# Kernel tuning notes

Hardware: AMD Instinct MI355X
Metric: run time of the kernel (lower is better)

The kernel has to match this reference:

```python
import jax, jax.numpy as jnp
import numpy as np

NUM_HEAD = 16
NUM_SEQ = 2048
NUM_FEAT = 1024
HEAD_DIM = NUM_FEAT // NUM_HEAD
LN_EPS = 1e-5


def _constants():
    # decay per head: log(1 - 2^{-5-h})
    decay = jnp.log(1.0 - 2.0 ** (-5.0 - jnp.arange(NUM_HEAD, dtype=jnp.float32)))
    idx = jnp.arange(NUM_SEQ, dtype=jnp.float32)
    diff = idx[:, None] - idx[None, :]                      # [s, s]
    # exp(diff * decay) on lower triangle (incl. diagonal), 0 above
    mask = jnp.where(diff[None] >= 0, jnp.exp(diff[None] * decay[:, None, None]), 0.0)  # [h, s, s]
    # rotary angles: each frequency repeated twice
    angle = 1.0 / 10000.0 ** jnp.linspace(0.0, 1.0, HEAD_DIM // 2)
    angle = jnp.repeat(angle, 2)                            # [hd]
    sin = jnp.sin(idx[:, None] * angle[None, :])            # [s, hd]
    cos = jnp.cos(idx[:, None] * angle[None, :])
    return mask, sin, cos


def _rotate_every_two(x):
    x1 = x[..., ::2]
    x2 = x[..., 1::2]
    return jnp.stack((-x2, x1), axis=-1).reshape(x.shape)


def setup_inputs() -> dict:
    key = jax.random.key(0)
    ks = jax.random.split(key, 5)
    b, s, d = 4, NUM_SEQ, NUM_FEAT
    x = jax.random.normal(ks[0], (b, s, d), dtype=jnp.float32)
    Wq = jax.random.normal(ks[1], (d, d), dtype=jnp.float32) * 0.02
    Wk = jax.random.normal(ks[2], (d, d), dtype=jnp.float32) * 0.02
    Wv = jax.random.normal(ks[3], (d, d), dtype=jnp.float32) * 0.02
    Wo = jax.random.normal(ks[4], (d, d), dtype=jnp.float32) * 0.02
    ln_w = jnp.ones((HEAD_DIM,), dtype=jnp.float32)
    ln_b = jnp.zeros((HEAD_DIM,), dtype=jnp.float32)
    return {"x": x, "Wq": Wq, "Wk": Wk, "Wv": Wv, "Wo": Wo, "ln_w": ln_w, "ln_b": ln_b}


def reference(x, Wq, Wk, Wv, Wo, ln_w, ln_b):
    b, s, d = x.shape
    h, hd = NUM_HEAD, HEAD_DIM
    mask, sin, cos = _constants()

    def proj(W):
        # torch Linear (no bias): x @ W.T -> [b, h, s, hd]
        return (x @ W.T).reshape(b, s, h, hd).transpose(0, 2, 1, 3)

    q, k, v = proj(Wq), proj(Wk), proj(Wv)
    # rotary theta shift (sin/cos broadcast over batch & head)
    q = q * cos + _rotate_every_two(q) * sin
    k = k * cos + _rotate_every_two(k) * sin

    r = jnp.einsum('bhsd,bhtd->bhst', q, k) * mask[None]    # decay-masked scores
    o = jnp.einsum('bhst,bhtd->bhsd', r, v)                 # [b, h, s, hd]

    # LayerNorm over head_dim
    mu = jnp.mean(o, axis=-1, keepdims=True)
    var = jnp.var(o, axis=-1, keepdims=True)
    y = (o - mu) * jax.lax.rsqrt(var + LN_EPS) * ln_w + ln_b

    y = y.transpose(0, 2, 1, 3).reshape(b, s, d)
    return jax.nn.silu(y) @ Wo.T
```

## Files before the change

### kernel.cpp

```cpp
#include <hip/hip_runtime.h>
#include <math.h>

typedef unsigned short u16;
typedef __attribute__((ext_vector_type(8))) short short8;
typedef __attribute__((ext_vector_type(4))) float floatx4;

#define LDS_AS(p) ((__attribute__((address_space(3))) void*)(p))
#define GLB_AS(p) ((const __attribute__((address_space(1))) void*)(p))

__device__ __forceinline__ u16 f2bf(float f) {
  unsigned int u = __float_as_uint(f);
  u += 0x7fffu + ((u >> 16) & 1u);
  return (u16)(u >> 16);
}

__device__ __forceinline__ void gld16(const void* g, void* l) {
  __builtin_amdgcn_global_load_lds(GLB_AS(g), LDS_AS(l), 16, 0, 0);
}

__device__ __forceinline__ floatx4 mfma16(short8 a, short8 b, floatx4 c) {
  return __builtin_amdgcn_mfma_f32_16x16x32_bf16(a, b, c, 0, 0, 0);
}

__global__ void prep_kernel(const float* __restrict__ x, const float* __restrict__ Wq,
                            const float* __restrict__ Wk, const float* __restrict__ Wv,
                            const float* __restrict__ Wo, u16* __restrict__ xbf,
                            u16* __restrict__ wqkv, u16* __restrict__ wo,
                            float2* __restrict__ rtab) {
  int i = blockIdx.x * blockDim.x + threadIdx.x;
  const int str = gridDim.x * blockDim.x;
  for (; i < 3211264; i += str) {
    if (i < 3145728) {
      const float* s; u16* d; int j;
      if (i < 2097152)      { s = x;  d = xbf;            j = i; }
      else if (i < 2359296) { s = Wq; d = wqkv;           j = i - 2097152; }
      else if (i < 2621440) { s = Wk; d = wqkv + 1048576; j = i - 2359296; }
      else if (i < 2883584) { s = Wv; d = wqkv + 2097152; j = i - 2621440; }
      else                  { s = Wo; d = wo;             j = i - 2883584; }
      float4 v = ((const float4*)s)[j];
      ushort4 o;
      o.x = f2bf(v.x); o.y = f2bf(v.y); o.z = f2bf(v.z); o.w = f2bf(v.w);
      ((ushort4*)d)[j] = o;
    } else {
      const int t = i - 3145728;
      const int seq = t >> 5, dh = t & 31;
      const float freq = exp2f(-(float)dh * 0.42863594770f);
      float sn, cs;
      __sincosf((float)seq * freq, &sn, &cs);
      rtab[t] = make_float2(sn, cs);
    }
  }
}

template <int EPI>
__global__ __launch_bounds__(512, 4)
void gemm_bt(const u16* __restrict__ A, const u16* __restrict__ Bw, int K,
             u16* __restrict__ qb, u16* __restrict__ kb, u16* __restrict__ vtb,
             u16* __restrict__ kwt, const float2* __restrict__ rtab,
             float* __restrict__ outp) {
  __shared__ __align__(16) u16 smem[36864];
  const int tid = threadIdx.x;
  const int w = tid >> 6, lane = tid & 63;
  const int quad = lane >> 4, l15 = lane & 15;
  const int wr = w >> 2, wc = w & 3;
  const int m0 = blockIdx.y * 128, n0 = blockIdx.x * 256;

  const u16* Ag = A + (size_t)(m0 + w * 16 + l15) * K + quad * 8;
  const u16* Bg = Bw + (size_t)(n0 + 2 * w * 16 + l15) * K + quad * 8;
  const size_t row16 = (size_t)16 * K;

  auto stage = [&](int buf, int k0) {
    const int nb = buf * 12288;
    gld16(Ag + k0, &smem[nb + w * 512]);
#pragma unroll
    for (int e = 0; e < 2; ++e)
      gld16(Bg + e * row16 + k0, &smem[nb + 4096 + (2 * w + e) * 512]);
  };

  floatx4 acc[4][4] = {};
  const int NT = K >> 5;

  stage(0, 0);
  stage(1, 32);

  int cur = 0, stg = 2;
  for (int t = 0; t < NT; ++t) {
    if (t + 1 < NT)
      asm volatile("s_waitcnt vmcnt(3)" ::: "memory");
    else
      asm volatile("s_waitcnt vmcnt(0)" ::: "memory");
    __builtin_amdgcn_s_barrier();
    asm volatile("" ::: "memory");
    __builtin_amdgcn_sched_barrier(0);

    if (t + 2 < NT) stage(stg, (t + 2) * 32);

    const u16* Ap = &smem[cur * 12288];
    const u16* Bp = &smem[cur * 12288 + 4096];
    short8 a[4], b[4];
#pragma unroll
    for (int i = 0; i < 4; ++i)
      a[i] = *(const short8*)&Ap[(wr * 4 + i) * 512 + lane * 8];
#pragma unroll
    for (int j = 0; j < 4; ++j)
      b[j] = *(const short8*)&Bp[(wc * 4 + j) * 512 + lane * 8];
    __builtin_amdgcn_s_setprio(1);
#pragma unroll
    for (int i = 0; i < 4; ++i)
#pragma unroll
      for (int j = 0; j < 4; ++j)
        acc[i][j] = mfma16(a[i], b[j], acc[i][j]);
    __builtin_amdgcn_s_setprio(0);
    asm volatile("" ::: "memory");
    cur = (cur == 2) ? 0 : cur + 1;
    stg = (stg == 2) ? 0 : stg + 1;
  }
  __builtin_amdgcn_s_barrier();

  u16* scr = &smem[w * 4096];

  const int mrb = m0 + wr * 64;
  const int ncb = n0 + wc * 64;

  if (EPI == 0) {
    const int which = n0 >> 10;
    const int c1024 = ncb & 1023;
    const int bidx = mrb >> 11;
    const int hh = c1024 >> 6;
    const int seq0 = mrb & 2047;
    const int lr = lane >> 3, lc = lane & 7;

    if (which < 2) {
#pragma unroll
      for (int j = 0; j < 4; ++j) {
        const int d = j * 16 + l15;
        const int dc = d >> 3, dl = d & 7;
#pragma unroll
        for (int i = 0; i < 4; ++i)
#pragma unroll
          for (int r = 0; r < 4; ++r) {
            const int sl = i * 16 + quad * 4 + r;
            const int seq = seq0 + sl;
            const float v = acc[i][j][r];
            const float p = __shfl_xor(v, 1, 64);
            const float2 sc = rtab[(d >> 1) + seq * 32];
            const float res = (d & 1) ? (v * sc.y + p * sc.x) : (v * sc.y - p * sc.x);
            scr[sl * 64 + (((dc + (sl >> 2)) & 7) << 3) + dl] = f2bf(res);
          }
      }
      u16* dst = ((which == 0) ? qb : kb) + (size_t)(bidx * 16 + hh) * 131072 +
                 (size_t)seq0 * 64;
#pragma unroll
      for (int cch = 0; cch < 8; ++cch) {
        const int row = cch * 8 + lr;
        const int slot = (lc + (row >> 2)) & 7;
        short8 vv = *(const short8*)&scr[row * 64 + slot * 8];
        *(short8*)(dst + (size_t)row * 64 + lc * 8) = vv;
      }
      if (which == 1) {
        const float l2h = __log2f(1.0f - exp2f(-(float)(5 + hh)));
#pragma unroll
        for (int j = 0; j < 4; ++j) {
          const int d = j * 16 + l15;
#pragma unroll
          for (int i = 0; i < 4; ++i) {
            ushort4 pk;
#pragma unroll
            for (int r = 0; r < 4; ++r) {
              const int sl = i * 16 + quad * 4 + r;
              const int seq = seq0 + sl;
              const float v = acc[i][j][r];
              const float p = __shfl_xor(v, 1, 64);
              const float2 sc = rtab[(d >> 1) + seq * 32];
              const float res = (d & 1) ? (v * sc.y + p * sc.x) : (v * sc.y - p * sc.x);
              const float wgt = exp2f((float)(127 - (seq & 127)) * l2h);
              ((u16*)&pk)[r] = f2bf(res * wgt);
            }
            *(ushort4*)&scr[d * 64 + ((i * 16 + quad * 4 + 8 * (d & 7)) & 63)] = pk;
          }
        }
        u16* dw = kwt + (size_t)(bidx * 16 + hh) * 131072 + seq0;
#pragma unroll
        for (int cch = 0; cch < 8; ++cch) {
          const int drow = cch * 8 + lr;
          const int slot = (lc + (drow & 7)) & 7;
          short8 vv = *(const short8*)&scr[drow * 64 + slot * 8];
          *(short8*)(dw + (size_t)drow * 2048 + lc * 8) = vv;
        }
      }
    } else {
#pragma unroll
      for (int j = 0; j < 4; ++j) {
        const int d = j * 16 + l15;
#pragma unroll
        for (int i = 0; i < 4; ++i) {
          ushort4 pk;
          pk.x = f2bf(acc[i][j][0]);
          pk.y = f2bf(acc[i][j][1]);
          pk.z = f2bf(acc[i][j][2]);
          pk.w = f2bf(acc[i][j][3]);
          *(ushort4*)&scr[d * 64 + ((i * 16 + quad * 4 + 8 * (d & 7)) & 63)] = pk;
        }
      }
      u16* dh = vtb + (size_t)(bidx * 16 + hh) * 131072 + seq0;
#pragma unroll
      for (int cch = 0; cch < 8; ++cch) {
        const int drow = cch * 8 + lr;
        const int slot = (lc + (drow & 7)) & 7;
        short8 vv = *(const short8*)&scr[drow * 64 + slot * 8];
        *(short8*)(dh + (size_t)drow * 2048 + lc * 8) = vv;
      }
    }
  } else {
    float* scrf = (float*)scr;
    const int lr4 = lane >> 4, lc16 = lane & 15;
#pragma unroll
    for (int p = 0; p < 4; ++p) {
#pragma unroll
      for (int j = 0; j < 4; ++j)
#pragma unroll
        for (int r = 0; r < 4; ++r)
          scrf[(quad * 4 + r) * 65 + j * 16 + l15] = acc[p][j][r];
#pragma unroll
      for (int cch = 0; cch < 4; ++cch) {
        const int rr = cch * 4 + lr4;
        float4 vv = *(const float4*)&scrf[rr * 65 + lc16 * 4];
        *(float4*)&outp[(size_t)(mrb + p * 16 + rr) * 1024 + ncb + lc16 * 4] = vv;
      }
    }
  }
}

__global__ __launch_bounds__(256, 4)
void kvchunk_kernel(const u16* __restrict__ kwt, const u16* __restrict__ vtb,
                    float* __restrict__ U) {
  __shared__ __align__(16) u16 kls[16 * 512];
  __shared__ __align__(16) u16 vls[16 * 512];
  const int c = blockIdx.x, bh = blockIdx.y;
  const int tid = threadIdx.x, w = tid >> 6, lane = tid & 63;
  const int quad = lane >> 4, l15 = lane & 15;
  const u16* kg = kwt + (size_t)bh * 131072 + c * 128;
  const u16* vg = vtb + (size_t)bh * 131072 + c * 128;
#pragma unroll
  for (int rg = 0; rg < 4; ++rg) {
    const int rid = w * 4 + rg;
    const int m = rid >> 2, kst = rid & 3;
    gld16(kg + (size_t)(m * 16 + l15) * 2048 + kst * 32 + quad * 8, &kls[rid * 512]);
    gld16(vg + (size_t)(m * 16 + l15) * 2048 + kst * 32 + quad * 8, &vls[rid * 512]);
  }
  __syncthreads();
  floatx4 acc[4] = {};
#pragma unroll
  for (int kst = 0; kst < 4; ++kst) {
    short8 bf = *(const short8*)&vls[(w * 4 + kst) * 512 + lane * 8];
#pragma unroll
    for (int m = 0; m < 4; ++m) {
      short8 af = *(const short8*)&kls[(m * 4 + kst) * 512 + lane * 8];
      acc[m] = mfma16(af, bf, acc[m]);
    }
  }
  float* Ub = U + ((size_t)bh * 16 + c) * 4096;
#pragma unroll
  for (int m = 0; m < 4; ++m)
#pragma unroll
    for (int r = 0; r < 4; ++r)
      Ub[(m * 16 + quad * 4 + r) * 64 + w * 16 + l15] = acc[m][r];
}

__global__ void scan_kernel(const float* __restrict__ U, u16* __restrict__ Sb) {
  const int bh = blockIdx.x;
  const int w = threadIdx.x >> 6, l = threadIdx.x & 63;
  const int h = bh & 15;
  const float l2 = __log2f(1.0f - exp2f(-(float)(5 + h)));
  const float lamL = exp2f(128.0f * l2);
  float S[16];
#pragma unroll
  for (int i = 0; i < 16; ++i) S[i] = 0.f;
  for (int c = 0; c < 16; ++c) {
    u16* sp = Sb + ((size_t)bh * 16 + c) * 4096 + l * 64 + w * 16;
#pragma unroll
    for (int dk = 0; dk < 16; dk += 4) {
      ushort4 pk;
      pk.x = f2bf(S[dk]);     pk.y = f2bf(S[dk + 1]);
      pk.z = f2bf(S[dk + 2]); pk.w = f2bf(S[dk + 3]);
      *(ushort4*)&sp[dk] = pk;
    }
    const float* up = U + ((size_t)bh * 16 + c) * 4096 + (w * 16) * 64 + l;
#pragma unroll
    for (int dk = 0; dk < 16; ++dk)
      S[dk] = lamL * S[dk] + up[dk * 64];
  }
}

__global__ __launch_bounds__(256, 2)
void attn_chunk_kernel(const u16* __restrict__ qb, const u16* __restrict__ kb,
                       const u16* __restrict__ vtb, const u16* __restrict__ Sb,
                       const float* __restrict__ lnw, const float* __restrict__ lnb,
                       u16* __restrict__ yb) {
  __shared__ __align__(16) u16 kls[16 * 512];
  __shared__ __align__(16) u16 vls[16 * 512];
  __shared__ __align__(16) u16 Sls[8 * 512];
  __shared__ __align__(16) u16 pls[4 * 32 * 40];

  const int c = blockIdx.x, bh = blockIdx.y, h = bh & 15;
  const int tid = threadIdx.x;
  const int w = tid >> 6, lane = tid & 63, quad = lane >> 4, l15 = lane & 15;
  const float l2 = __log2f(1.0f - exp2f(-(float)(5 + h)));

  const u16* kg = kb + (size_t)bh * 131072 + (size_t)c * 128 * 64;
  const u16* vg = vtb + (size_t)bh * 131072 + (size_t)c * 128;
  const u16* Sg = Sb + ((size_t)bh * 16 + c) * 4096;
#pragma unroll
  for (int rg = 0; rg < 4; ++rg) {
    const int kid = w * 4 + rg;
    const int nsub = kid >> 1, kk = kid & 1;
    gld16(kg + (size_t)(nsub * 16 + l15) * 64 + kk * 32 + quad * 8, &kls[kid * 512]);
    const int jd = kid >> 2, kst = kid & 3;
    gld16(vg + (size_t)(jd * 16 + l15) * 2048 + kst * 32 + quad * 8, &vls[kid * 512]);
  }
#pragma unroll
  for (int e = 0; e < 2; ++e) {
    const int rid = w * 2 + e;
    const int nd = rid >> 1, kk = rid & 1;
    gld16(Sg + (size_t)(nd * 16 + l15) * 64 + kk * 32 + quad * 8, &Sls[rid * 512]);
  }

  short8 qf[2][2];
  {
    const u16* qbase = qb + ((size_t)bh * 2048 + c * 128 + w * 32 + l15) * 64 + quad * 8;
#pragma unroll
    for (int i = 0; i < 2; ++i)
#pragma unroll
      for (int kk = 0; kk < 2; ++kk)
        qf[i][kk] = *(const short8*)(qbase + (size_t)i * 16 * 64 + kk * 32);
  }
  float lnwv[4], lnbv[4];
#pragma unroll
  for (int jd = 0; jd < 4; ++jd) {
    lnwv[jd] = lnw[jd * 16 + l15];
    lnbv[jd] = lnb[jd * 16 + l15];
  }
  __syncthreads();

  floatx4 sacc[2][8] = {};
#pragma unroll
  for (int kk = 0; kk < 2; ++kk) {
    short8 bf[8];
#pragma unroll
    for (int j = 0; j < 8; ++j)
      bf[j] = *(const short8*)&kls[(j * 2 + kk) * 512 + lane * 8];
#pragma unroll
    for (int i = 0; i < 2; ++i)
#pragma unroll
      for (int j = 0; j < 8; ++j)
        sacc[i][j] = mfma16(qf[i][kk], bf[j], sacc[i][j]);
  }

  floatx4 oacc[2][4] = {};
#pragma unroll
  for (int kk = 0; kk < 2; ++kk)
#pragma unroll
    for (int nd = 0; nd < 4; ++nd) {
      short8 sf = *(const short8*)&Sls[(nd * 2 + kk) * 512 + lane * 8];
#pragma unroll
      for (int i = 0; i < 2; ++i)
        oacc[i][nd] = mfma16(qf[i][kk], sf, oacc[i][nd]);
    }
  float rowf[8];
#pragma unroll
  for (int i = 0; i < 2; ++i)
#pragma unroll
    for (int r = 0; r < 4; ++r)
      rowf[i * 4 + r] = exp2f((float)(w * 32 + i * 16 + quad * 4 + r) * l2);
  const float lam1 = exp2f(l2);
#pragma unroll
  for (int i = 0; i < 2; ++i)
#pragma unroll
    for (int nd = 0; nd < 4; ++nd)
#pragma unroll
      for (int r = 0; r < 4; ++r)
        oacc[i][nd][r] *= rowf[i * 4 + r] * lam1;

  float colf[8];
#pragma unroll
  for (int j = 0; j < 8; ++j) colf[j] = exp2f(-(float)(j * 16 + l15) * l2);
  u16* pw = &pls[w * 1280];
#pragma unroll
  for (int kst = 0; kst < 4; ++kst) {
#pragma unroll
    for (int jl = 0; jl < 2; ++jl) {
      const int j = kst * 2 + jl;
#pragma unroll
      for (int i = 0; i < 2; ++i)
#pragma unroll
        for (int r = 0; r < 4; ++r) {
          const int srow = i * 16 + quad * 4 + r;
          const int dlt = (w * 32 + srow) - (j * 16 + l15);
          const float v =
              (dlt >= 0) ? sacc[i][j][r] * rowf[i * 4 + r] * colf[j] : 0.0f;
          pw[srow * 40 + jl * 16 + l15] = f2bf(v);
        }
    }
    short8 pf[2], vf[4];
#pragma unroll
    for (int i = 0; i < 2; ++i)
      pf[i] = *(const short8*)&pw[(i * 16 + l15) * 40 + quad * 8];
#pragma unroll
    for (int jd = 0; jd < 4; ++jd)
      vf[jd] = *(const short8*)&vls[(jd * 4 + kst) * 512 + lane * 8];
#pragma unroll
    for (int i = 0; i < 2; ++i)
#pragma unroll
      for (int jd = 0; jd < 4; ++jd)
        oacc[i][jd] = mfma16(pf[i], vf[jd], oacc[i][jd]);
  }

  const int b = bh >> 4;
#pragma unroll
  for (int i = 0; i < 2; ++i)
#pragma unroll
    for (int r = 0; r < 4; ++r) {
      float sum = 0.f, ssq = 0.f;
#pragma unroll
      for (int jd = 0; jd < 4; ++jd) {
        const float v = oacc[i][jd][r];
        sum += v;
        ssq += v * v;
      }
#pragma unroll
      for (int off = 1; off < 16; off <<= 1) {
        sum += __shfl_xor(sum, off, 64);
        ssq += __shfl_xor(ssq, off, 64);
      }
      const float mu = sum * (1.0f / 64.0f);
      const float var = ssq * (1.0f / 64.0f) - mu * mu;
      const float rst = rsqrtf(var + 1e-5f);
      const int sg = c * 128 + w * 32 + i * 16 + quad * 4 + r;
      u16* dst = yb + ((size_t)b * 2048 + sg) * 1024 + h * 64;
#pragma unroll
      for (int jd = 0; jd < 4; ++jd) {
        const float z = (oacc[i][jd][r] - mu) * rst * lnwv[jd] + lnbv[jd];
        const float y = z / (1.0f + expf(-z));
        dst[jd * 16 + l15] = f2bf(y);
      }
    }
}

extern "C" void kernel_launch(void* const* d_in, const int* in_sizes, int n_in,
                              void* d_out, int out_size, void* d_ws, size_t ws_size,
                              hipStream_t stream) {
  const float* x   = (const float*)d_in[0];
  const float* Wq  = (const float*)d_in[1];
  const float* Wk  = (const float*)d_in[2];
  const float* Wv  = (const float*)d_in[3];
  const float* Wo  = (const float*)d_in[4];
  const float* lnw = (const float*)d_in[5];
  const float* lnb = (const float*)d_in[6];
  float* out = (float*)d_out;

  char* ws = (char*)d_ws;
  u16* xbf  = (u16*)(ws + 0);
  u16* wqkv = (u16*)(ws + 16777216);
  u16* Sb   = (u16*)(ws + 16777216);
  u16* qbuf = (u16*)(ws + 25165824);
  u16* kbuf = (u16*)(ws + 41943040);
  u16* vtb  = (u16*)(ws + 58720256);
  u16* wo   = (u16*)(ws + 75497472);
  float2* rtab = (float2*)(ws + 77594624);
  u16* yb   = xbf;
  u16* kwt  = (u16*)d_out;
  float* Ubuf = (float*)((char*)d_out + 16777216);

  prep_kernel<<<dim3(1024), dim3(256), 0, stream>>>(x, Wq, Wk, Wv, Wo, xbf, wqkv, wo,
                                                    rtab);
  gemm_bt<0><<<dim3(12, 64), dim3(512), 0, stream>>>(xbf, wqkv, 1024, qbuf, kbuf, vtb,
                                                     kwt, rtab, nullptr);
  kvchunk_kernel<<<dim3(16, 64), dim3(256), 0, stream>>>(kwt, vtb, Ubuf);
  scan_kernel<<<dim3(64), dim3(256), 0, stream>>>(Ubuf, Sb);
  attn_chunk_kernel<<<dim3(16, 64), dim3(256), 0, stream>>>(qbuf, kbuf, vtb, Sb, lnw,
                                                            lnb, yb);
  gemm_bt<1><<<dim3(4, 64), dim3(512), 0, stream>>>(yb, wo, 1024, nullptr, nullptr,
                                                    nullptr, nullptr, nullptr, out);
}
```

Baseline: 273.3 us.

## Pre-tile GEMM operands into MFMA fragment layout for contiguous async loads

The prep kernel now writes x and the weights in bf16 in a tiled layout where each 16-row by 32-column fragment is stored contiguously in lane order. The GEMM stage loads each fragment as one contiguous 1KB chunk instead of strided row reads. The retention kernel's output is staged through swizzled LDS and written in the same tiled layout, so the output projection GEMM can read it the same way. This removes strided global access in the GEMM loads, at the cost of more complex index math in prep and an extra LDS round trip plus a barrier in the epilogue.

```diff
diff --git a/kernel.cpp b/kernel.cpp
--- a/kernel.cpp
+++ b/kernel.cpp
@@ -24,23 +24,33 @@
 
 __global__ void prep_kernel(const float* __restrict__ x, const float* __restrict__ Wq,
                             const float* __restrict__ Wk, const float* __restrict__ Wv,
-                            const float* __restrict__ Wo, u16* __restrict__ xbf,
-                            u16* __restrict__ wqkv, u16* __restrict__ wo,
+                            const float* __restrict__ Wo, u16* __restrict__ xp,
+                            u16* __restrict__ wqkvp, u16* __restrict__ wop,
                             float2* __restrict__ rtab) {
   int i = blockIdx.x * blockDim.x + threadIdx.x;
   const int str = gridDim.x * blockDim.x;
   for (; i < 3211264; i += str) {
     if (i < 3145728) {
-      const float* s; u16* d; int j;
-      if (i < 2097152)      { s = x;  d = xbf;            j = i; }
-      else if (i < 2359296) { s = Wq; d = wqkv;           j = i - 2097152; }
-      else if (i < 2621440) { s = Wk; d = wqkv + 1048576; j = i - 2359296; }
-      else if (i < 2883584) { s = Wv; d = wqkv + 2097152; j = i - 2621440; }
-      else                  { s = Wo; d = wo;             j = i - 2883584; }
-      float4 v = ((const float4*)s)[j];
+      int U; u16* d;
+      const float* s;
+      if (i < 2097152)      { U = i;           d = xp;    s = x;  }
+      else if (i < 2883584) { U = i - 2097152; d = wqkvp; s = nullptr; }
+      else                  { U = i - 2883584; d = wop;   s = Wo; }
+      const int tile = U >> 12;
+      const int kc   = (U >> 7) & 31;
+      const int lane = (U >> 1) & 63;
+      const int jh   = U & 1;
+      const int scol = kc * 32 + (lane >> 4) * 8 + jh * 4;
+      int srow = tile * 16 + (lane & 15);
+      if (s == nullptr) {
+        const int sel = srow >> 10;
+        srow &= 1023;
+        s = (sel == 0) ? Wq : (sel == 1) ? Wk : Wv;
+      }
+      float4 v = ((const float4*)s)[srow * 256 + (scol >> 2)];
       ushort4 o;
       o.x = f2bf(v.x); o.y = f2bf(v.y); o.z = f2bf(v.z); o.w = f2bf(v.w);
-      ((ushort4*)d)[j] = o;
+      ((ushort4*)d)[U] = o;
     } else {
       const int t = i - 3145728;
       const int seq = t >> 5, dh = t & 31;
@@ -65,23 +75,23 @@
   const int wr = w >> 2, wc = w & 3;
   const int m0 = blockIdx.y * 128, n0 = blockIdx.x * 256;
 
-  const u16* Ag = A + (size_t)(m0 + w * 16 + l15) * K + quad * 8;
-  const u16* Bg = Bw + (size_t)(n0 + 2 * w * 16 + l15) * K + quad * 8;
-  const size_t row16 = (size_t)16 * K;
-
-  auto stage = [&](int buf, int k0) {
+  const size_t tsz = (size_t)(K >> 5) * 512;
+  const u16* Apk = A + ((size_t)(m0 >> 4) + w) * tsz + lane * 8;
+  const u16* B0  = Bw + ((size_t)(n0 >> 4) + 2 * w) * tsz + lane * 8;
+  const u16* B1  = B0 + tsz;
+
+  auto stage = [&](int buf, int kc) {
     const int nb = buf * 12288;
-    gld16(Ag + k0, &smem[nb + w * 512]);
-#pragma unroll
-    for (int e = 0; e < 2; ++e)
-      gld16(Bg + e * row16 + k0, &smem[nb + 4096 + (2 * w + e) * 512]);
+    gld16(Apk + (size_t)kc * 512, &smem[nb + w * 512]);
+    gld16(B0 + (size_t)kc * 512, &smem[nb + 4096 + (2 * w) * 512]);
+    gld16(B1 + (size_t)kc * 512, &smem[nb + 4096 + (2 * w + 1) * 512]);
   };
 
   floatx4 acc[4][4] = {};
   const int NT = K >> 5;
 
   stage(0, 0);
-  stage(1, 32);
+  stage(1, 1);
 
   int cur = 0, stg = 2;
   for (int t = 0; t < NT; ++t) {
@@ -93,7 +103,7 @@
     asm volatile("" ::: "memory");
     __builtin_amdgcn_sched_barrier(0);
 
-    if (t + 2 < NT) stage(stg, (t + 2) * 32);
+    if (t + 2 < NT) stage(stg, t + 2);
 
     const u16* Ap = &smem[cur * 12288];
     const u16* Bp = &smem[cur * 12288 + 4096];
@@ -415,6 +425,8 @@
         oacc[i][jd] = mfma16(pf[i], vf[jd], oacc[i][jd]);
   }
 
+  __syncthreads();
+  u16* scrw = &kls[w * 2048];
   const int b = bh >> 4;
 #pragma unroll
   for (int i = 0; i < 2; ++i)
@@ -435,14 +447,24 @@
       const float mu = sum * (1.0f / 64.0f);
       const float var = ssq * (1.0f / 64.0f) - mu * mu;
       const float rst = rsqrtf(var + 1e-5f);
-      const int sg = c * 128 + w * 32 + i * 16 + quad * 4 + r;
-      u16* dst = yb + ((size_t)b * 2048 + sg) * 1024 + h * 64;
+      const int sl = i * 16 + quad * 4 + r;
 #pragma unroll
       for (int jd = 0; jd < 4; ++jd) {
         const float z = (oacc[i][jd][r] - mu) * rst * lnwv[jd] + lnbv[jd];
         const float y = z / (1.0f + expf(-z));
-        dst[jd * 16 + l15] = f2bf(y);
-      }
+        const int f = jd * 16 + l15;
+        scrw[sl * 64 + ((((f >> 3) + (sl >> 2)) & 7) << 3) + (f & 7)] = f2bf(y);
+      }
+    }
+  const int tile0 = b * 128 + c * 8 + w * 2;
+#pragma unroll
+  for (int tt = 0; tt < 2; ++tt)
+#pragma unroll
+    for (int kcl = 0; kcl < 2; ++kcl) {
+      const int row = tt * 16 + l15;
+      const int slot = ((kcl * 4 + quad) + (row >> 2)) & 7;
+      short8 vv = *(const short8*)&scrw[row * 64 + slot * 8];
+      *(short8*)(yb + ((size_t)(tile0 + tt) * 32 + h * 2 + kcl) * 512 + lane * 8) = vv;
     }
 }
 
```

New measurement: 240.7 us. 11.9% less time.
